# Optimization experiments

Hardware: AMD Instinct MI355X
Metric: run time of the kernel (lower is better)

The kernel has to match this reference:

```python
import jax, jax.numpy as jnp
import numpy as np

N_NODES = 50000
N_EDGES = 800000
IN_CH = 128
HEADS = 4
HEAD_DIM = 32  # out_channels // heads = 128 // 4
OUT_CH = HEADS * HEAD_DIM
NEG_SLOPE = 0.2
LN_EPS = 1e-5


def setup_inputs() -> dict:
    key = jax.random.key(0)
    ks = jax.random.split(key, 10)
    s = 1.0 / np.sqrt(IN_CH)
    return {
        "x": jax.random.normal(ks[0], (N_NODES, IN_CH), jnp.float32),
        "edge_index": jax.random.randint(ks[1], (2, N_EDGES), 0, N_NODES, dtype=jnp.int64),
        "W_l": jax.random.normal(ks[2], (IN_CH, OUT_CH), jnp.float32) * s,
        "b_l": jnp.zeros((OUT_CH,), jnp.float32),
        "W_r": jax.random.normal(ks[3], (IN_CH, OUT_CH), jnp.float32) * s,
        "b_r": jnp.zeros((OUT_CH,), jnp.float32),
        "att": jax.random.normal(ks[4], (HEADS, HEAD_DIM), jnp.float32) * (1.0 / np.sqrt(HEAD_DIM)),
        "bias": jnp.zeros((OUT_CH,), jnp.float32),
        "gamma": jnp.ones((OUT_CH,), jnp.float32),
        "beta": jnp.zeros((OUT_CH,), jnp.float32),
    }


def reference(x, edge_index, W_l, b_l, W_r, b_r, att, bias, gamma, beta):
    N = x.shape[0]
    H, C = att.shape
    # add self loops (PyG GATv2Conv default add_self_loops=True)
    loops = jnp.arange(N, dtype=edge_index.dtype)
    src = jnp.concatenate([edge_index[0], loops])  # source j
    dst = jnp.concatenate([edge_index[1], loops])  # target i
    # separate source/target transforms (share_weights=False)
    xl = (x @ W_l + b_l).reshape(N, H, C)  # source features
    xr = (x @ W_r + b_r).reshape(N, H, C)  # target features
    # GATv2 attention: e_ij = att . leaky_relu(xl_j + xr_i)
    e = xl[src] + xr[dst]                              # [E', H, C]
    e = jnp.where(e > 0, e, NEG_SLOPE * e)             # leaky_relu(0.2)
    score = jnp.einsum('ehc,hc->eh', e, att)           # [E', H]
    # segment softmax over edges sharing the same destination node
    smax = jax.ops.segment_max(score, dst, num_segments=N)      # [N, H]
    score = jnp.exp(score - smax[dst])
    denom = jax.ops.segment_sum(score, dst, num_segments=N)     # [N, H]
    alpha = score / denom[dst]                                   # [E', H]
    # weighted scatter-sum of source messages
    msg = alpha[:, :, None] * xl[src]                            # [E', H, C]
    out = jax.ops.segment_sum(msg, dst, num_segments=N)          # [N, H, C]
    out = out.reshape(N, H * C) + bias
    # SiLU
    out = out * jax.nn.sigmoid(out)
    # LayerNorm over feature dim
    mu = jnp.mean(out, axis=-1, keepdims=True)
    var = jnp.mean(jnp.square(out - mu), axis=-1, keepdims=True)
    out = (out - mu) * jax.lax.rsqrt(var + LN_EPS) * gamma + beta
    return out
```

## Files before the change

kernel.cpp:

```cpp
#include <hip/hip_runtime.h>
#include <hip/hip_fp16.h>
#include <math.h>

#define CH 128
#define NEG_SLOPE 0.2f
#define LN_EPS 1e-5f
#define CAP 64

typedef _Float16 f16;
typedef _Float16 f16x2 __attribute__((ext_vector_type(2)));
typedef _Float16 f16x4 __attribute__((ext_vector_type(4)));
typedef _Float16 f16x8 __attribute__((ext_vector_type(8)));
typedef float    f32x4 __attribute__((ext_vector_type(4)));

__device__ __forceinline__ f16x2 u2h(unsigned u) {
    union { unsigned u; f16x2 h; } v; v.u = u; return v.h;
}

__global__ void k_init(const float* __restrict__ Wl, const float* __restrict__ Wr,
                       f16* __restrict__ Wt, int* __restrict__ cnt, int N)
{
    int tid = blockIdx.x * 256 + threadIdx.x;
    if (tid < 256 * CH) {
        int k   = tid >> 8;
        int col = tid & 255;
        float w = (col < CH) ? Wl[k * CH + col] : Wr[k * CH + (col - CH)];
        Wt[(size_t)col * CH + k] = (f16)w;
    }
    if (tid < N) cnt[tid] = 0;
}

__global__ __launch_bounds__(256) void k_transform(
    const float* __restrict__ x, const f16* __restrict__ Wt,
    const float* __restrict__ bl, const float* __restrict__ br,
    f16* __restrict__ xlh, f16* __restrict__ xrh, int N)
{
    const int wave = (blockIdx.x * 256 + threadIdx.x) >> 6;
    const int lane = threadIdx.x & 63;
    const int m0   = wave * 16;
    if (m0 >= N) return;

    const int n16  = lane & 15;
    const int quad = lane >> 4;

    f16x8 xfr[4];
    {
        int mrow = m0 + n16; if (mrow >= N) mrow = N - 1;
        const float* xrow = x + (size_t)mrow * CH + quad * 8;
#pragma unroll
        for (int ks = 0; ks < 4; ++ks) {
            float4 p0 = *(const float4*)(xrow + ks * 32);
            float4 p1 = *(const float4*)(xrow + ks * 32 + 4);
            f16x8 f; f[0] = (f16)p0.x; f[1] = (f16)p0.y; f[2] = (f16)p0.z; f[3] = (f16)p0.w;
                     f[4] = (f16)p1.x; f[5] = (f16)p1.y; f[6] = (f16)p1.z; f[7] = (f16)p1.w;
            xfr[ks] = f;
        }
    }

#pragma unroll
    for (int ct = 0; ct < 16; ++ct) {
        f32x4 acc = {0.f, 0.f, 0.f, 0.f};
        const int acol = ct * 16 + n16;
        const f16* wp = Wt + (size_t)acol * CH + quad * 8;
#pragma unroll
        for (int ks = 0; ks < 4; ++ks) {
            f16x8 afr = *(const f16x8*)(wp + ks * 32);
            acc = __builtin_amdgcn_mfma_f32_16x16x32_f16(afr, xfr[ks], acc, 0, 0, 0);
        }
        const int node = m0 + n16;
        const int chq  = ct * 16 + quad * 4;
        if (node < N) {
            if (ct < 8) {
                float4 bv = *(const float4*)&bl[chq];
                f16x4 pk = {(f16)(acc[0] + bv.x), (f16)(acc[1] + bv.y),
                            (f16)(acc[2] + bv.z), (f16)(acc[3] + bv.w)};
                *(f16x4*)(xlh + (size_t)node * CH + chq) = pk;
            } else {
                int cc = chq - CH;
                float4 bv = *(const float4*)&br[cc];
                f16x4 pk = {(f16)(acc[0] + bv.x), (f16)(acc[1] + bv.y),
                            (f16)(acc[2] + bv.z), (f16)(acc[3] + bv.w)};
                *(f16x4*)(xrh + (size_t)node * CH + cc) = pk;
            }
        }
    }
}

#define FILL_EPB 4096
__global__ __launch_bounds__(256) void k_fill(
    const int* __restrict__ ei, int E, unsigned CM,
    int* __restrict__ cnt, int* __restrict__ col)
{
    const int cls = blockIdx.x & 7;
    const int sl  = blockIdx.x >> 3;
    const int base = sl * FILL_EPB + threadIdx.x * 4;

#pragma unroll
    for (int i = 0; i < 4; ++i) {
        int e = base + i * 1024;
        if (e < E) {
            int4 dv = *(const int4*)&ei[E + e];
            int4 sv = *(const int4*)&ei[e];
            int dd[4] = {dv.x, dv.y, dv.z, dv.w};
            int ss[4] = {sv.x, sv.y, sv.z, sv.w};
#pragma unroll
            for (int k = 0; k < 4; ++k) {
                int d = dd[k];
                if ((int)__umulhi((unsigned)d, CM) == cls) {
                    int pos = atomicAdd(&cnt[d], 1);
                    if (pos < CAP) col[((size_t)d << 6) + pos] = ss[k];
                }
            }
        }
    }
}

__global__ __launch_bounds__(256) void k_aggregate(
    const f16* __restrict__ xlh, const f16* __restrict__ xrh,
    const int* __restrict__ col, const int* __restrict__ cnt,
    const float* __restrict__ att, const float* __restrict__ bias,
    const float* __restrict__ gamma, const float* __restrict__ beta,
    float* __restrict__ out, int N)
{
    const int wid  = __builtin_amdgcn_readfirstlane(threadIdx.x >> 6);
    const int lane = threadIdx.x & 63;
    const int n    = blockIdx.x * 4 + wid;
    if (n >= N) return;

    const int l16 = lane & 15;
    const int g   = lane >> 4;
    const int c0  = l16 * 8;

    const int start = n << 6;
    int cn = cnt[n]; cn = cn < CAP ? cn : CAP;
    const int total = cn + 1;

    f16x8 xr8, at8;
    {
        xr8 = *(const f16x8*)(xrh + (size_t)n * CH + c0);
        float4 a0 = *(const float4*)&att[c0];
        float4 a1 = *(const float4*)&att[c0 + 4];
        const float L2E = 1.44269504f;
        at8[0]=(f16)(a0.x*L2E); at8[1]=(f16)(a0.y*L2E);
        at8[2]=(f16)(a0.z*L2E); at8[3]=(f16)(a0.w*L2E);
        at8[4]=(f16)(a1.x*L2E); at8[5]=(f16)(a1.y*L2E);
        at8[6]=(f16)(a1.z*L2E); at8[7]=(f16)(a1.w*L2E);
    }
    const f16x8 c02 = {(f16)NEG_SLOPE,(f16)NEG_SLOPE,(f16)NEG_SLOPE,(f16)NEG_SLOPE,
                       (f16)NEG_SLOPE,(f16)NEG_SLOPE,(f16)NEG_SLOPE,(f16)NEG_SLOPE};

    float l_run = 0.f;
    float acc[8] = {0.f,0.f,0.f,0.f,0.f,0.f,0.f,0.f};

    for (int t0 = 0; t0 < total; t0 += 4) {
        const int base = start + t0 - 1;
        int s0 = (t0 == 0) ? n : col[base];
        int s1 = col[base + 1];
        int s2 = col[base + 2];
        int s3 = col[base + 3];
        int src = (g == 0) ? s0 : ((g == 1) ? s1 : ((g == 2) ? s2 : s3));
        unsigned su = (unsigned)src;
        su = (su < (unsigned)N) ? su : 0u;

        f16x8 u = *(const f16x8*)(xlh + ((size_t)su << 7) + c0);
        f16x8 tt = u + xr8;
        f16x8 lk = __builtin_elementwise_max(tt, tt * c02);
        union { f16x8 v; f16x2 h[4]; } L, A;
        L.v = lk; A.v = at8;
        float s = __builtin_amdgcn_fdot2(L.h[0], A.h[0], 0.f, false);
        s = __builtin_amdgcn_fdot2(L.h[1], A.h[1], s, false);
        s = __builtin_amdgcn_fdot2(L.h[2], A.h[2], s, false);
        s = __builtin_amdgcn_fdot2(L.h[3], A.h[3], s, false);
        int t;
        t = __builtin_amdgcn_update_dpp(0, __builtin_bit_cast(int, s), 0xB1, 0xF, 0xF, false);
        s += __builtin_bit_cast(float, t);
        t = __builtin_amdgcn_update_dpp(0, __builtin_bit_cast(int, s), 0x4E, 0xF, 0xF, false);
        s += __builtin_bit_cast(float, t);
        float w;
        asm("v_exp_f32 %0, %1" : "=v"(w) : "v"(s));
        w = (t0 + g < total) ? w : 0.f;
        l_run += w;
#pragma unroll
        for (int j = 0; j < 8; ++j) acc[j] += (float)u[j] * w;
    }

    l_run += __shfl_xor(l_run, 16);
    l_run += __shfl_xor(l_run, 32);
#pragma unroll
    for (int j = 0; j < 8; ++j) {
        acc[j] += __shfl_xor(acc[j], 16);
        acc[j] += __shfl_xor(acc[j], 32);
    }

    const float inv = 1.f / l_run;
    float4 b0 = *(const float4*)&bias[c0];
    float4 b1 = *(const float4*)&bias[c0 + 4];
    float y[8];
    y[0] = acc[0]*inv + b0.x; y[1] = acc[1]*inv + b0.y;
    y[2] = acc[2]*inv + b0.z; y[3] = acc[3]*inv + b0.w;
    y[4] = acc[4]*inv + b1.x; y[5] = acc[5]*inv + b1.y;
    y[6] = acc[6]*inv + b1.z; y[7] = acc[7]*inv + b1.w;
    float s1 = 0.f, s2 = 0.f;
#pragma unroll
    for (int j = 0; j < 8; ++j) {
        y[j] = y[j] / (1.f + __expf(-y[j]));
        s1 += y[j];
        s2 += y[j] * y[j];
    }
#pragma unroll
    for (int off = 1; off < 16; off <<= 1) {
        s1 += __shfl_xor(s1, off);
        s2 += __shfl_xor(s2, off);
    }
    float mu   = s1 * (1.f / 128.f);
    float var  = s2 * (1.f / 128.f) - mu * mu;
    float rstd = rsqrtf(var + LN_EPS);
    float4 g0 = *(const float4*)&gamma[c0];
    float4 g1 = *(const float4*)&gamma[c0 + 4];
    float4 e0 = *(const float4*)&beta[c0];
    float4 e1 = *(const float4*)&beta[c0 + 4];
    float4 o0, o1;
    o0.x = (y[0]-mu)*rstd*g0.x + e0.x;  o0.y = (y[1]-mu)*rstd*g0.y + e0.y;
    o0.z = (y[2]-mu)*rstd*g0.z + e0.z;  o0.w = (y[3]-mu)*rstd*g0.w + e0.w;
    o1.x = (y[4]-mu)*rstd*g1.x + e1.x;  o1.y = (y[5]-mu)*rstd*g1.y + e1.y;
    o1.z = (y[6]-mu)*rstd*g1.z + e1.z;  o1.w = (y[7]-mu)*rstd*g1.w + e1.w;
    if (g == 0) {
        float* orow = out + (size_t)n * CH + c0;
        *(float4*)orow       = o0;
        *(float4*)(orow + 4) = o1;
    }
}

extern "C" void kernel_launch(void* const* d_in, const int* in_sizes, int n_in,
                              void* d_out, int out_size, void* d_ws, size_t ws_size,
                              hipStream_t stream)
{
    const float* x    = (const float*)d_in[0];
    const int*   ei   = (const int*)  d_in[1];
    const float* Wl   = (const float*)d_in[2];
    const float* bl   = (const float*)d_in[3];
    const float* Wr   = (const float*)d_in[4];
    const float* br   = (const float*)d_in[5];
    const float* att  = (const float*)d_in[6];
    const float* bias = (const float*)d_in[7];
    const float* gam  = (const float*)d_in[8];
    const float* bet  = (const float*)d_in[9];
    float* out = (float*)d_out;

    const int N = in_sizes[0] / CH;
    const int E = in_sizes[1] / 2;

    char* ws = (char*)d_ws;
    size_t off = 0;
    auto carve = [&](size_t bytes) -> char* {
        char* p = ws + off;
        off += (bytes + 255) & ~(size_t)255;
        return p;
    };
    f16* xlh  = (f16*)carve((size_t)N * CH * sizeof(f16));
    f16* xrh  = (f16*)carve((size_t)N * CH * sizeof(f16));
    f16* Wt   = (f16*)carve((size_t)256 * CH * sizeof(f16));
    int* cnt  = (int*)carve((size_t)N * sizeof(int));
    int* col  = (int*)carve(((size_t)N * CAP + 16) * sizeof(int));
    (void)ws_size;

    const int nwaves = (N + 15) / 16;
    const int TB     = (nwaves * 64 + 255) / 256;
    const int IB     = (((N > 256 * CH ? N : 256 * CH) + 255) / 256);

    const unsigned CM = (unsigned)(((8ULL << 32) + (unsigned)N - 1) / (unsigned)N);
    const int S  = (E + FILL_EPB - 1) / FILL_EPB;
    const int FB = 8 * S;

    k_init      <<<IB, 256, 0, stream>>>(Wl, Wr, Wt, cnt, N);
    k_transform <<<TB, 256, 0, stream>>>(x, Wt, bl, br, xlh, xrh, N);
    k_fill      <<<FB, 256, 0, stream>>>(ei, E, CM, cnt, col);
    k_aggregate <<<(N + 3) / 4, 256, 0, stream>>>(xlh, xrh, col, cnt,
                                                  att, bias, gam, bet, out, N);
}
```

Baseline: 217.1 us.

## Process two nodes per wave in aggregation with prefetched neighbor indices

The aggregation kernel now gives each 64-lane wave two destination nodes, with 32 lanes per node and two edges in flight per iteration. Previously one node used the whole wave with four edge groups. The self-loop is handled once before the loop, and the next neighbor index is prefetched to hide the index-load latency. The goal is less idle lane work on low-degree nodes and a shorter shuffle reduction. In exchange, each wave loops up to the larger of its two nodes' degrees, so the shorter node's lanes sit idle for the extra iterations.

```diff
diff --git a/kernel.cpp b/kernel.cpp
--- a/kernel.cpp
+++ b/kernel.cpp
@@ -12,10 +12,6 @@
 typedef _Float16 f16x4 __attribute__((ext_vector_type(4)));
 typedef _Float16 f16x8 __attribute__((ext_vector_type(8)));
 typedef float    f32x4 __attribute__((ext_vector_type(4)));
-
-__device__ __forceinline__ f16x2 u2h(unsigned u) {
-    union { unsigned u; f16x2 h; } v; v.u = u; return v.h;
-}
 
 __global__ void k_init(const float* __restrict__ Wl, const float* __restrict__ Wr,
                        f16* __restrict__ Wt, int* __restrict__ cnt, int N)
@@ -122,18 +118,22 @@
     const float* __restrict__ gamma, const float* __restrict__ beta,
     float* __restrict__ out, int N)
 {
-    const int wid  = __builtin_amdgcn_readfirstlane(threadIdx.x >> 6);
     const int lane = threadIdx.x & 63;
-    const int n    = blockIdx.x * 4 + wid;
-    if (n >= N) return;
-
-    const int l16 = lane & 15;
-    const int g   = lane >> 4;
-    const int c0  = l16 * 8;
-
-    const int start = n << 6;
+    const int wid  = threadIdx.x >> 6;
+    const int nsub = lane >> 5;
+    const int g    = (lane >> 4) & 1;
+    const int l16  = lane & 15;
+    const int c0   = l16 * 8;
+
+    const int nraw = blockIdx.x * 8 + wid * 2 + nsub;
+    if (blockIdx.x * 8 >= N) return;
+    const int n  = (nraw < N) ? nraw : N - 1;
+    const int n6 = n << 6;
+
     int cn = cnt[n]; cn = cn < CAP ? cn : CAP;
-    const int total = cn + 1;
+    const int cnA = __builtin_amdgcn_readlane(cn, 0);
+    const int cnB = __builtin_amdgcn_readlane(cn, 32);
+    const int cmax = cnA > cnB ? cnA : cnB;
 
     f16x8 xr8, at8;
     {
@@ -152,16 +152,34 @@
     float l_run = 0.f;
     float acc[8] = {0.f,0.f,0.f,0.f,0.f,0.f,0.f,0.f};
 
-    for (int t0 = 0; t0 < total; t0 += 4) {
-        const int base = start + t0 - 1;
-        int s0 = (t0 == 0) ? n : col[base];
-        int s1 = col[base + 1];
-        int s2 = col[base + 2];
-        int s3 = col[base + 3];
-        int src = (g == 0) ? s0 : ((g == 1) ? s1 : ((g == 2) ? s2 : s3));
-        unsigned su = (unsigned)src;
+    {
+        f16x8 u = *(const f16x8*)(xlh + ((size_t)n << 7) + c0);
+        f16x8 tt = u + xr8;
+        f16x8 lk = __builtin_elementwise_max(tt, tt * c02);
+        union { f16x8 v; f16x2 h[4]; } L, A;
+        L.v = lk; A.v = at8;
+        float s = __builtin_amdgcn_fdot2(L.h[0], A.h[0], 0.f, false);
+        s = __builtin_amdgcn_fdot2(L.h[1], A.h[1], s, false);
+        s = __builtin_amdgcn_fdot2(L.h[2], A.h[2], s, false);
+        s = __builtin_amdgcn_fdot2(L.h[3], A.h[3], s, false);
+        int t;
+        t = __builtin_amdgcn_update_dpp(0, __builtin_bit_cast(int, s), 0xB1, 0xF, 0xF, false);
+        s += __builtin_bit_cast(float, t);
+        t = __builtin_amdgcn_update_dpp(0, __builtin_bit_cast(int, s), 0x4E, 0xF, 0xF, false);
+        s += __builtin_bit_cast(float, t);
+        float w;
+        asm("v_exp_f32 %0, %1" : "=v"(w) : "v"(s));
+        w = (g == 0) ? w : 0.f;
+        l_run = w;
+#pragma unroll
+        for (int j = 0; j < 8; ++j) acc[j] = (float)u[j] * w;
+    }
+
+    int idx = col[n6 + g];
+    for (int t0 = 0; t0 < cmax; t0 += 2) {
+        int nidx = col[n6 + t0 + 2 + g];
+        unsigned su = (unsigned)idx;
         su = (su < (unsigned)N) ? su : 0u;
-
         f16x8 u = *(const f16x8*)(xlh + ((size_t)su << 7) + c0);
         f16x8 tt = u + xr8;
         f16x8 lk = __builtin_elementwise_max(tt, tt * c02);
@@ -178,53 +196,50 @@
         s += __builtin_bit_cast(float, t);
         float w;
         asm("v_exp_f32 %0, %1" : "=v"(w) : "v"(s));
-        w = (t0 + g < total) ? w : 0.f;
+        w = (t0 + g < cn) ? w : 0.f;
         l_run += w;
 #pragma unroll
         for (int j = 0; j < 8; ++j) acc[j] += (float)u[j] * w;
+        idx = nidx;
     }
 
     l_run += __shfl_xor(l_run, 16);
-    l_run += __shfl_xor(l_run, 32);
-#pragma unroll
-    for (int j = 0; j < 8; ++j) {
-        acc[j] += __shfl_xor(acc[j], 16);
-        acc[j] += __shfl_xor(acc[j], 32);
-    }
-
-    const float inv = 1.f / l_run;
-    float4 b0 = *(const float4*)&bias[c0];
-    float4 b1 = *(const float4*)&bias[c0 + 4];
-    float y[8];
-    y[0] = acc[0]*inv + b0.x; y[1] = acc[1]*inv + b0.y;
-    y[2] = acc[2]*inv + b0.z; y[3] = acc[3]*inv + b0.w;
-    y[4] = acc[4]*inv + b1.x; y[5] = acc[5]*inv + b1.y;
-    y[6] = acc[6]*inv + b1.z; y[7] = acc[7]*inv + b1.w;
-    float s1 = 0.f, s2 = 0.f;
-#pragma unroll
-    for (int j = 0; j < 8; ++j) {
-        y[j] = y[j] / (1.f + __expf(-y[j]));
-        s1 += y[j];
-        s2 += y[j] * y[j];
-    }
-#pragma unroll
-    for (int off = 1; off < 16; off <<= 1) {
-        s1 += __shfl_xor(s1, off);
-        s2 += __shfl_xor(s2, off);
-    }
-    float mu   = s1 * (1.f / 128.f);
-    float var  = s2 * (1.f / 128.f) - mu * mu;
-    float rstd = rsqrtf(var + LN_EPS);
-    float4 g0 = *(const float4*)&gamma[c0];
-    float4 g1 = *(const float4*)&gamma[c0 + 4];
-    float4 e0 = *(const float4*)&beta[c0];
-    float4 e1 = *(const float4*)&beta[c0 + 4];
-    float4 o0, o1;
-    o0.x = (y[0]-mu)*rstd*g0.x + e0.x;  o0.y = (y[1]-mu)*rstd*g0.y + e0.y;
-    o0.z = (y[2]-mu)*rstd*g0.z + e0.z;  o0.w = (y[3]-mu)*rstd*g0.w + e0.w;
-    o1.x = (y[4]-mu)*rstd*g1.x + e1.x;  o1.y = (y[5]-mu)*rstd*g1.y + e1.y;
-    o1.z = (y[6]-mu)*rstd*g1.z + e1.z;  o1.w = (y[7]-mu)*rstd*g1.w + e1.w;
-    if (g == 0) {
+#pragma unroll
+    for (int j = 0; j < 8; ++j) acc[j] += __shfl_xor(acc[j], 16);
+
+    if (g == 0 && nraw < N) {
+        const float inv = 1.f / l_run;
+        float4 b0 = *(const float4*)&bias[c0];
+        float4 b1 = *(const float4*)&bias[c0 + 4];
+        float y[8];
+        y[0] = acc[0]*inv + b0.x; y[1] = acc[1]*inv + b0.y;
+        y[2] = acc[2]*inv + b0.z; y[3] = acc[3]*inv + b0.w;
+        y[4] = acc[4]*inv + b1.x; y[5] = acc[5]*inv + b1.y;
+        y[6] = acc[6]*inv + b1.z; y[7] = acc[7]*inv + b1.w;
+        float s1 = 0.f, s2 = 0.f;
+#pragma unroll
+        for (int j = 0; j < 8; ++j) {
+            y[j] = y[j] / (1.f + __expf(-y[j]));
+            s1 += y[j];
+            s2 += y[j] * y[j];
+        }
+#pragma unroll
+        for (int off = 1; off < 16; off <<= 1) {
+            s1 += __shfl_xor(s1, off);
+            s2 += __shfl_xor(s2, off);
+        }
+        float mu   = s1 * (1.f / 128.f);
+        float var  = s2 * (1.f / 128.f) - mu * mu;
+        float rstd = rsqrtf(var + LN_EPS);
+        float4 g0 = *(const float4*)&gamma[c0];
+        float4 g1 = *(const float4*)&gamma[c0 + 4];
+        float4 e0 = *(const float4*)&beta[c0];
+        float4 e1 = *(const float4*)&beta[c0 + 4];
+        float4 o0, o1;
+        o0.x = (y[0]-mu)*rstd*g0.x + e0.x;  o0.y = (y[1]-mu)*rstd*g0.y + e0.y;
+        o0.z = (y[2]-mu)*rstd*g0.z + e0.z;  o0.w = (y[3]-mu)*rstd*g0.w + e0.w;
+        o1.x = (y[4]-mu)*rstd*g1.x + e1.x;  o1.y = (y[5]-mu)*rstd*g1.y + e1.y;
+        o1.z = (y[6]-mu)*rstd*g1.z + e1.z;  o1.w = (y[7]-mu)*rstd*g1.w + e1.w;
         float* orow = out + (size_t)n * CH + c0;
         *(float4*)orow       = o0;
         *(float4*)(orow + 4) = o1;
@@ -275,6 +290,6 @@
     k_init      <<<IB, 256, 0, stream>>>(Wl, Wr, Wt, cnt, N);
     k_transform <<<TB, 256, 0, stream>>>(x, Wt, bl, br, xlh, xrh, N);
     k_fill      <<<FB, 256, 0, stream>>>(ei, E, CM, cnt, col);
-    k_aggregate <<<(N + 3) / 4, 256, 0, stream>>>(xlh, xrh, col, cnt,
+    k_aggregate <<<(N + 7) / 8, 256, 0, stream>>>(xlh, xrh, col, cnt,
                                                   att, bias, gam, bet, out, N);
 }
```

Result: no change. 214.1 us (-1.4%).
